# Kernel tuning notes

Measured on AMD Instinct MI355X. Metric: run time of the kernel, lower is better.

## Reference

```python
import jax, jax.numpy as jnp
import numpy as np

MUL0, MUL1, SCALARS_OUT = 16, 16, 128
L0, L1 = MUL0, MUL1 * 3            # 16, 48
PATH_NUMEL = MUL0 * MUL1 * SCALARS_OUT  # 32768 per path, two paths
EPS = 1e-5
# e3nn normalization: irrep_normalization='component' -> alpha = dim(ir_out) = 1;
# path_normalization='element' -> divide by sum over paths to same output of mul1*mul2 = 256+256 = 512.
PATH_COEFF = 1.0 / np.sqrt(512.0)
CG_110 = 1.0 / np.sqrt(3.0)  # wigner_3j(1,1,0)[i,j] = delta_ij/sqrt(3) (unit Frobenius norm)


def layer_norm(x, g, b):
    mu = jnp.mean(x, axis=-1, keepdims=True)
    var = jnp.mean(jnp.square(x - mu), axis=-1, keepdims=True)
    return (x - mu) * jax.lax.rsqrt(var + EPS) * g + b


def ff_block(x, g, b, w1, w2, b2):
    # LayerNorm -> Linear(no bias) -> SiLU -> Linear(bias); residual=False in both uses
    h = jax.nn.silu(layer_norm(x, g, b) @ w1)
    return h @ w2 + b2


def setup_inputs() -> dict:
    key = jax.random.key(0)
    ks = jax.random.split(key, 8)
    N = 2048
    return {
        "x": jax.random.normal(ks[0], (N, L0 + L1), dtype=jnp.float32),
        "we_ln_g": jnp.ones((L0,), jnp.float32),
        "we_ln_b": jnp.zeros((L0,), jnp.float32),
        "we_w1": jax.random.normal(ks[1], (L0, 4 * L0), jnp.float32) / np.sqrt(L0),
        "we_w2": jax.random.normal(ks[2], (4 * L0, 2 * PATH_NUMEL), jnp.float32) / np.sqrt(4 * L0),
        "we_b2": jnp.zeros((2 * PATH_NUMEL,), jnp.float32),
        "om_ln_g": jnp.ones((SCALARS_OUT,), jnp.float32),
        "om_ln_b": jnp.zeros((SCALARS_OUT,), jnp.float32),
        "om_w1": jax.random.normal(ks[3], (SCALARS_OUT, 4 * SCALARS_OUT), jnp.float32) / np.sqrt(SCALARS_OUT),
        "om_w2": jax.random.normal(ks[4], (4 * SCALARS_OUT, 1), jnp.float32) / np.sqrt(4 * SCALARS_OUT),
        "om_b2": jnp.zeros((1,), jnp.float32),
    }


def reference(x, we_ln_g, we_ln_b, we_w1, we_w2, we_b2,
              om_ln_g, om_ln_b, om_w1, om_w2, om_b2):
    N = x.shape[0]
    feats = x[:, :L0]                       # [N, 16] scalars (0e)
    x1 = x[:, L0:].reshape(N, MUL1, 3)      # [N, 16, 3] vectors (1o)

    # per-sample tensor-product weights (shared_weights=False)
    w = ff_block(feats, we_ln_g, we_ln_b, we_w1, we_w2, we_b2)  # [N, 65536]
    w0 = w[:, :PATH_NUMEL].reshape(N, MUL0, MUL0, SCALARS_OUT)
    w1 = w[:, PATH_NUMEL:].reshape(N, MUL1, MUL1, SCALARS_OUT)

    # path 0: 0e x 0e -> 0e  (uvw)
    o0 = jnp.einsum('nu,nv,nuvw->nw', feats, feats, w0)
    # path 1: 1o x 1o -> 0e  (uvw, CG = delta_ij/sqrt(3))
    o1 = jnp.einsum('nui,nvi,nuvw->nw', x1, x1, w1) * CG_110
    tp_out = PATH_COEFF * (o0 + o1)          # [N, 128]

    return ff_block(tp_out, om_ln_g, om_ln_b, om_w1, om_w2, om_b2)  # [N, 1]
```

## Files before the change

### kernel.cpp

```cpp
#include <hip/hip_runtime.h>
#include <hip/hip_bf16.h>
#include <cstdint>

#define EPS 1e-5f
#define PATH_COEFF 0.04419417382415922f
#define CG110     0.5773502691896258f

typedef __bf16 v8bf __attribute__((ext_vector_type(8)));
typedef float  v4f  __attribute__((ext_vector_type(4)));
typedef _Float16 v4h __attribute__((ext_vector_type(4)));

static __device__ __forceinline__ unsigned short f2bf(float x){
    unsigned int u = __builtin_bit_cast(unsigned int, x);
    u += 0x7fffu + ((u >> 16) & 1u);
    return (unsigned short)(u >> 16);
}
static __device__ __forceinline__ unsigned short f2h(float x){
    return __builtin_bit_cast(unsigned short, (_Float16)x);
}

__global__ __launch_bounds__(256)
void k_pre(const float* __restrict__ w2, const float* __restrict__ b2,
           unsigned short* __restrict__ Vt2,
           const float* __restrict__ om_w1, unsigned short* __restrict__ w1t,
           const float* __restrict__ x, const float* __restrict__ lng,
           const float* __restrict__ lnb, const float* __restrict__ we_w1,
           unsigned short* __restrict__ Q2, float* __restrict__ Ht, int N)
{
    __shared__ __align__(16) unsigned short tile[32][128];
    int b = blockIdx.x;
    int t = threadIdx.x;

    if (b < 260){
        int k    = b >> 2;
        int slab = b & 3;
        const float* srcbase = (k < 64) ? (w2 + (size_t)k * 65536) : b2;
        for (int chunk = 0; chunk < 4; ++chunk){
            int pbase = slab*128 + chunk*32;
            #pragma unroll
            for (int i = 0; i < 4; ++i){
                int g = t + 256*i;
                int ploc = g >> 5, c4 = g & 31;
                const float4 v = *(const float4*)(srcbase + (size_t)(pbase + ploc)*128 + c4*4);
                unsigned int w0 = (unsigned)f2bf(v.x) | ((unsigned)f2bf(v.y) << 16);
                unsigned int w1 = (unsigned)f2bf(v.z) | ((unsigned)f2bf(v.w) << 16);
                *(uint2*)&tile[ploc][c4*4] = make_uint2(w0, w1);
            }
            __syncthreads();
            int w = t & 127, h = t >> 7;
            int ps = slab*4 + chunk;
            unsigned int words[8];
            #pragma unroll
            for (int g2 = 0; g2 < 8; ++g2)
                words[g2] = (unsigned)tile[h*16 + g2*2][w] | ((unsigned)tile[h*16 + g2*2 + 1][w] << 16);
            unsigned short* dq0 = Vt2 + (((size_t)(k*16 + ps)*4 + 2*h    )*128 + w)*8;
            unsigned short* dq1 = Vt2 + (((size_t)(k*16 + ps)*4 + 2*h + 1)*128 + w)*8;
            *(uint4*)dq0 = make_uint4(words[0], words[1], words[2], words[3]);
            *(uint4*)dq1 = make_uint4(words[4], words[5], words[6], words[7]);
            __syncthreads();
        }
    } else if (b < 264){
        int j0 = (b - 260) * 128;
        for (int chunk = 0; chunk < 4; ++chunk){
            #pragma unroll
            for (int i = 0; i < 4; ++i){
                int g = t + 256*i;
                int wloc = g >> 5, c4 = g & 31;
                int w = chunk*32 + wloc;
                const float4 v = *(const float4*)(om_w1 + (size_t)w*512 + j0 + c4*4);
                unsigned int a = (unsigned)f2bf(v.x) | ((unsigned)f2bf(v.y) << 16);
                unsigned int bb = (unsigned)f2bf(v.z) | ((unsigned)f2bf(v.w) << 16);
                *(uint2*)&tile[wloc][c4*4] = make_uint2(a, bb);
            }
            __syncthreads();
            int jl = t & 127, h = t >> 7;
            unsigned int words[8];
            #pragma unroll
            for (int g2 = 0; g2 < 8; ++g2)
                words[g2] = (unsigned)tile[h*16 + g2*2][jl] | ((unsigned)tile[h*16 + g2*2 + 1][jl] << 16);
            unsigned short* dst = w1t + (size_t)(j0 + jl)*128 + chunk*32 + h*16;
            *(uint4*)dst       = make_uint4(words[0], words[1], words[2], words[3]);
            *(uint4*)(dst + 8) = make_uint4(words[4], words[5], words[6], words[7]);
            __syncthreads();
        }
    } else {
        int wv = t >> 6, lane = t & 63;
        int row = (b - 264)*4 + wv;
        const float* xr = x + (size_t)row * 64;
        float f[16]; float mu = 0.f;
        #pragma unroll
        for (int u = 0; u < 16; ++u){ f[u] = xr[u]; mu += f[u]; }
        mu *= (1.f/16.f);
        float var = 0.f;
        #pragma unroll
        for (int u = 0; u < 16; ++u){ float d = f[u] - mu; var += d*d; }
        var *= (1.f/16.f);
        float inv = rsqrtf(var + EPS);
        float lnf[16];
        #pragma unroll
        for (int u = 0; u < 16; ++u) lnf[u] = (f[u]-mu)*inv*lng[u] + lnb[u];
        float h1 = 0.f;
        #pragma unroll
        for (int u = 0; u < 16; ++u) h1 += lnf[u] * we_w1[u*64 + lane];
        float h = h1 / (1.f + expf(-h1));
        Ht[(size_t)lane * N + row] = h;
        if (lane == 0) Ht[(size_t)64 * N + row] = 1.f;

        union { unsigned short qs[8]; uint4 v; } qu;
        #pragma unroll
        for (int j = 0; j < 8; ++j){
            int p = lane*8 + j;
            float q;
            if (p < 256){
                int u = p >> 4, v = p & 15;
                q = PATH_COEFF * f[u] * f[v];
            } else {
                int pp = p - 256;
                int u = pp >> 4, v = pp & 15;
                const float* ya = xr + 16 + u*3;
                const float* yb = xr + 16 + v*3;
                q = (PATH_COEFF * CG110) * (ya[0]*yb[0] + ya[1]*yb[1] + ya[2]*yb[2]);
            }
            qu.qs[j] = f2bf(q);
        }
        int rb = row >> 6, r64 = row & 63;
        int ps = lane >> 2, quad4 = lane & 3;
        *(uint4*)(Q2 + (((size_t)(rb*16 + ps)*4 + quad4)*64 + r64)*8) = qu.v;
    }
}

__global__ __launch_bounds__(256, 4)
void k_main(const unsigned short* __restrict__ Q2, const unsigned short* __restrict__ Vt2,
            const float* __restrict__ Ht, unsigned short* __restrict__ partial, int N)
{
    __shared__ __align__(16) unsigned short stile[4][64*72];
    int g = blockIdx.x & 7;
    int j = blockIdx.x >> 3;
    int kb, mb;
    if (j < 128){ mb = j >> 3; kb = g*8 + (j & 7); }
    else { if (g != 0) return; mb = j - 128; kb = 64; }

    int tid  = threadIdx.x;
    int lane = tid & 63, wv = tid >> 6;
    int r2 = wv >> 1, c2 = wv & 1;
    int quad = lane >> 4, l16 = lane & 15;
    int rowbase = mb*128 + r2*64;
    int rb = rowbase >> 6;
    int wbase = c2*64;

    const unsigned short* aroot = Q2  + (size_t)rb*32768 + quad*512  + l16*8;
    const unsigned short* broot = Vt2 + (size_t)kb*65536 + quad*1024 + (wbase + l16)*8;

    v4f acc[4][4];
    #pragma unroll
    for (int m=0;m<4;++m)
      #pragma unroll
      for (int n=0;n<4;++n)
        #pragma unroll
        for (int r=0;r<4;++r) acc[m][n][r] = 0.f;

    #pragma unroll 4
    for (int ps = 0; ps < 16; ++ps){
        const unsigned short* ap = aroot + ps*2048;
        const unsigned short* bp = broot + ps*4096;
        v8bf a[4], bb[4];
        #pragma unroll
        for (int m=0;m<4;++m) a[m]  = *(const v8bf*)(ap + m*128);
        #pragma unroll
        for (int n=0;n<4;++n) bb[n] = *(const v8bf*)(bp + n*128);
        #pragma unroll
        for (int m=0;m<4;++m)
          #pragma unroll
          for (int n=0;n<4;++n)
            acc[m][n] = __builtin_amdgcn_mfma_f32_16x16x32_bf16(a[m], bb[n], acc[m][n], 0, 0, 0);
    }

    const float* hp = Ht + (size_t)kb*N + rowbase + quad*4;
    unsigned short* my = stile[wv];
    #pragma unroll
    for (int m=0;m<4;++m){
        v4f hv = *(const v4f*)(hp + m*16);
        #pragma unroll
        for (int n=0;n<4;++n)
          #pragma unroll
          for (int r=0;r<4;++r)
            my[(m*16 + quad*4 + r)*72 + n*16 + l16] = f2h(hv[r]*acc[m][n][r]);
    }
    unsigned short* gp = partial + ((size_t)(mb*65 + kb))*16384
                                 + (size_t)(r2*64)*128 + wbase;
    #pragma unroll
    for (int i = 0; i < 8; ++i){
        int row = i*8 + (lane >> 3);
        int c16 = (lane & 7)*8;
        uint4 v = *(const uint4*)&my[row*72 + c16];
        *(uint4*)(gp + (size_t)row*128 + c16) = v;
    }
}

__global__ __launch_bounds__(128)
void k_red(const unsigned short* __restrict__ partial, const float* __restrict__ g,
           const float* __restrict__ b, unsigned short* __restrict__ lnf, int N)
{
    int t = threadIdx.x;
    int row = blockIdx.x * 8 + (t >> 4);
    int w8  = (t & 15) * 8;
    int mb  = row >> 7, rin = row & 127;

    const unsigned short* p0 = partial + (size_t)mb*65*16384 + (size_t)rin*128 + w8;

    float s[8];
    #pragma unroll
    for (int j = 0; j < 8; ++j) s[j] = 0.f;

    #pragma unroll 13
    for (int sl = 0; sl < 65; ++sl){
        uint4 raw = *(const uint4*)(p0 + (size_t)sl*16384);
        union { uint4 u; _Float16 h[8]; } cv; cv.u = raw;
        #pragma unroll
        for (int j = 0; j < 8; ++j) s[j] += (float)cv.h[j];
    }

    float sum = 0.f, sq = 0.f;
    #pragma unroll
    for (int j = 0; j < 8; ++j){ sum += s[j]; sq += s[j]*s[j]; }
    #pragma unroll
    for (int off = 8; off > 0; off >>= 1){
        sum += __shfl_xor(sum, off, 16);
        sq  += __shfl_xor(sq,  off, 16);
    }
    float mu  = sum * (1.f/128.f);
    float var = sq * (1.f/128.f) - mu*mu;
    float inv = rsqrtf(var + EPS);
    unsigned short o[8];
    #pragma unroll
    for (int j = 0; j < 8; ++j)
        o[j] = f2bf((s[j]-mu)*inv*g[w8+j] + b[w8+j]);
    *(uint4*)(lnf + (size_t)row*128 + w8) = *(uint4*)o;
}

__global__ __launch_bounds__(256)
void k_mlp2(const unsigned short* __restrict__ lnf, const unsigned short* __restrict__ w1t,
            const float* __restrict__ w2, const float* __restrict__ b2,
            float* __restrict__ out, int N)
{
    __shared__ float red2[4][32];
    int tid = threadIdx.x, lane = tid & 63, wv = tid >> 6;
    int quad = lane >> 4, l16 = lane & 15;
    int rowbase = blockIdx.x * 32;
    int jbase = wv * 128;

    v4f acc[2][8];
    #pragma unroll
    for (int m=0;m<2;++m)
      #pragma unroll
      for (int n=0;n<8;++n)
        #pragma unroll
        for (int r=0;r<4;++r) acc[m][n][r] = 0.f;

    #pragma unroll
    for (int ps = 0; ps < 4; ++ps){
        v8bf a[2], bb[8];
        #pragma unroll
        for (int m=0;m<2;++m)
            a[m]  = *(const v8bf*)(lnf + (size_t)(rowbase + m*16 + l16)*128 + ps*32 + quad*8);
        #pragma unroll
        for (int n=0;n<8;++n)
            bb[n] = *(const v8bf*)(w1t + (size_t)(jbase + n*16 + l16)*128 + ps*32 + quad*8);
        #pragma unroll
        for (int m=0;m<2;++m)
          #pragma unroll
          for (int n=0;n<8;++n)
            acc[m][n] = __builtin_amdgcn_mfma_f32_16x16x32_bf16(a[m], bb[n], acc[m][n], 0, 0, 0);
    }

    float w2v[8];
    #pragma unroll
    for (int n=0;n<8;++n) w2v[n] = w2[jbase + n*16 + l16];

    #pragma unroll
    for (int m=0;m<2;++m){
        #pragma unroll
        for (int r=0;r<4;++r){
            float s = 0.f;
            #pragma unroll
            for (int n=0;n<8;++n){
                float v = acc[m][n][r];
                s += (v / (1.f + expf(-v))) * w2v[n];
            }
            #pragma unroll
            for (int off=8; off>0; off>>=1) s += __shfl_xor(s, off, 16);
            if (l16 == 0) red2[wv][m*16 + quad*4 + r] = s;
        }
    }
    __syncthreads();
    if (tid < 32)
        out[rowbase + tid] = red2[0][tid] + red2[1][tid] + red2[2][tid] + red2[3][tid] + b2[0];
}

extern "C" void kernel_launch(void* const* d_in, const int* in_sizes, int n_in,
                              void* d_out, int out_size, void* d_ws, size_t ws_size,
                              hipStream_t stream)
{
    const float* x     = (const float*)d_in[0];
    const float* we_g  = (const float*)d_in[1];
    const float* we_b  = (const float*)d_in[2];
    const float* we_w1 = (const float*)d_in[3];
    const float* we_w2 = (const float*)d_in[4];
    const float* we_b2 = (const float*)d_in[5];
    const float* om_g  = (const float*)d_in[6];
    const float* om_b  = (const float*)d_in[7];
    const float* om_w1 = (const float*)d_in[8];
    const float* om_w2 = (const float*)d_in[9];
    const float* om_b2 = (const float*)d_in[10];

    int N  = in_sizes[0] / 64;

    char* ws = (char*)d_ws;
    size_t offV = 0;
    size_t szV  = (size_t)65*16*4*128*8*2;
    size_t offQ = offV + szV;
    size_t szQ  = (size_t)N*512*2;
    size_t offH = offQ + szQ;
    size_t szH  = (size_t)65*N*4;
    size_t offP = offH + szH;
    size_t szP  = (size_t)65*N*128*2;
    size_t offL = offP + szP;
    size_t szL  = (size_t)N*128*2;
    size_t offW = offL + szL;

    unsigned short* Vt2 = (unsigned short*)(ws + offV);
    unsigned short* Q2  = (unsigned short*)(ws + offQ);
    float* Ht           = (float*)(ws + offH);
    unsigned short* Par = (unsigned short*)(ws + offP);
    unsigned short* Lnf = (unsigned short*)(ws + offL);
    unsigned short* W1t = (unsigned short*)(ws + offW);
    float* out = (float*)d_out;

    hipLaunchKernelGGL(k_pre,  dim3(264 + N/4), dim3(256), 0, stream,
                       we_w2, we_b2, Vt2, om_w1, W1t, x, we_g, we_b, we_w1, Q2, Ht, N);
    hipLaunchKernelGGL(k_main, dim3(144*8),     dim3(256), 0, stream, Q2, Vt2, Ht, Par, N);
    hipLaunchKernelGGL(k_red,  dim3(N/8),       dim3(128), 0, stream, Par, om_g, om_b, Lnf, N);
    hipLaunchKernelGGL(k_mlp2, dim3(N/32),      dim3(256), 0, stream, Lnf, W1t, om_w2, om_b2, out, N);
}
```

Measured before the change: 137.9 us.

## Process two hidden units per k_main block to halve partial-sum traffic

Each k_main block now computes two k slices (two hidden units) with separate accumulators that share the same A fragments. It combines them with their Ht scales before writing a single fp16 partial, so the partial buffer and the k_red reduction shrink from 65 to 33 slices. This cuts global writes and reads of partials and reuses A loads. In exchange it doubles accumulator registers, lowers the occupancy target to 2 blocks, and launches fewer blocks.

```diff
diff --git a/kernel.cpp b/kernel.cpp
--- a/kernel.cpp
+++ b/kernel.cpp
@@ -129,16 +129,16 @@
     }
 }
 
-__global__ __launch_bounds__(256, 4)
+__global__ __launch_bounds__(256, 2)
 void k_main(const unsigned short* __restrict__ Q2, const unsigned short* __restrict__ Vt2,
             const float* __restrict__ Ht, unsigned short* __restrict__ partial, int N)
 {
     __shared__ __align__(16) unsigned short stile[4][64*72];
     int g = blockIdx.x & 7;
     int j = blockIdx.x >> 3;
-    int kb, mb;
-    if (j < 128){ mb = j >> 3; kb = g*8 + (j & 7); }
-    else { if (g != 0) return; mb = j - 128; kb = 64; }
+    int kg, mb;
+    if (j < 64){ mb = j >> 2; kg = g*4 + (j & 3); }
+    else { if (g != 0) return; mb = j - 64; kg = 32; }
 
     int tid  = threadIdx.x;
     int lane = tid & 63, wv = tid >> 6;
@@ -148,45 +148,61 @@
     int rb = rowbase >> 6;
     int wbase = c2*64;
 
-    const unsigned short* aroot = Q2  + (size_t)rb*32768 + quad*512  + l16*8;
-    const unsigned short* broot = Vt2 + (size_t)kb*65536 + quad*1024 + (wbase + l16)*8;
-
-    v4f acc[4][4];
+    int k0 = kg*2;
+    int k1 = (kg == 32) ? 64 : k0 + 1;
+    float sel = (kg == 32) ? 0.f : 1.f;
+
+    const unsigned short* aroot  = Q2  + (size_t)rb*32768 + quad*512  + l16*8;
+    const unsigned short* broot0 = Vt2 + (size_t)k0*65536 + quad*1024 + (wbase + l16)*8;
+    const unsigned short* broot1 = Vt2 + (size_t)k1*65536 + quad*1024 + (wbase + l16)*8;
+
+    v4f accA[4][4], accB[4][4];
     #pragma unroll
     for (int m=0;m<4;++m)
       #pragma unroll
       for (int n=0;n<4;++n)
         #pragma unroll
-        for (int r=0;r<4;++r) acc[m][n][r] = 0.f;
-
-    #pragma unroll 4
+        for (int r=0;r<4;++r){ accA[m][n][r] = 0.f; accB[m][n][r] = 0.f; }
+
+    #pragma unroll 2
     for (int ps = 0; ps < 16; ++ps){
-        const unsigned short* ap = aroot + ps*2048;
-        const unsigned short* bp = broot + ps*4096;
-        v8bf a[4], bb[4];
-        #pragma unroll
-        for (int m=0;m<4;++m) a[m]  = *(const v8bf*)(ap + m*128);
-        #pragma unroll
-        for (int n=0;n<4;++n) bb[n] = *(const v8bf*)(bp + n*128);
+        const unsigned short* ap  = aroot  + ps*2048;
+        const unsigned short* bp0 = broot0 + ps*4096;
+        const unsigned short* bp1 = broot1 + ps*4096;
+        v8bf a[4], b0[4], b1[4];
+        #pragma unroll
+        for (int m=0;m<4;++m) a[m]  = *(const v8bf*)(ap  + m*128);
+        #pragma unroll
+        for (int n=0;n<4;++n) b0[n] = *(const v8bf*)(bp0 + n*128);
+        #pragma unroll
+        for (int n=0;n<4;++n) b1[n] = *(const v8bf*)(bp1 + n*128);
         #pragma unroll
         for (int m=0;m<4;++m)
           #pragma unroll
           for (int n=0;n<4;++n)
-            acc[m][n] = __builtin_amdgcn_mfma_f32_16x16x32_bf16(a[m], bb[n], acc[m][n], 0, 0, 0);
-    }
-
-    const float* hp = Ht + (size_t)kb*N + rowbase + quad*4;
+            accA[m][n] = __builtin_amdgcn_mfma_f32_16x16x32_bf16(a[m], b0[n], accA[m][n], 0, 0, 0);
+        #pragma unroll
+        for (int m=0;m<4;++m)
+          #pragma unroll
+          for (int n=0;n<4;++n)
+            accB[m][n] = __builtin_amdgcn_mfma_f32_16x16x32_bf16(a[m], b1[n], accB[m][n], 0, 0, 0);
+    }
+
+    const float* hp0 = Ht + (size_t)k0*N + rowbase + quad*4;
+    const float* hp1 = Ht + (size_t)k1*N + rowbase + quad*4;
     unsigned short* my = stile[wv];
     #pragma unroll
     for (int m=0;m<4;++m){
-        v4f hv = *(const v4f*)(hp + m*16);
+        v4f h0 = *(const v4f*)(hp0 + m*16);
+        v4f h1 = *(const v4f*)(hp1 + m*16);
         #pragma unroll
         for (int n=0;n<4;++n)
           #pragma unroll
           for (int r=0;r<4;++r)
-            my[(m*16 + quad*4 + r)*72 + n*16 + l16] = f2h(hv[r]*acc[m][n][r]);
-    }
-    unsigned short* gp = partial + ((size_t)(mb*65 + kb))*16384
+            my[(m*16 + quad*4 + r)*72 + n*16 + l16] =
+                f2h(h0[r]*accA[m][n][r] + sel*h1[r]*accB[m][n][r]);
+    }
+    unsigned short* gp = partial + ((size_t)(mb*33 + kg))*16384
                                  + (size_t)(r2*64)*128 + wbase;
     #pragma unroll
     for (int i = 0; i < 8; ++i){
@@ -206,14 +222,14 @@
     int w8  = (t & 15) * 8;
     int mb  = row >> 7, rin = row & 127;
 
-    const unsigned short* p0 = partial + (size_t)mb*65*16384 + (size_t)rin*128 + w8;
+    const unsigned short* p0 = partial + (size_t)mb*33*16384 + (size_t)rin*128 + w8;
 
     float s[8];
     #pragma unroll
     for (int j = 0; j < 8; ++j) s[j] = 0.f;
 
-    #pragma unroll 13
-    for (int sl = 0; sl < 65; ++sl){
+    #pragma unroll 11
+    for (int sl = 0; sl < 33; ++sl){
         uint4 raw = *(const uint4*)(p0 + (size_t)sl*16384);
         union { uint4 u; _Float16 h[8]; } cv; cv.u = raw;
         #pragma unroll
@@ -323,7 +339,7 @@
     size_t offH = offQ + szQ;
     size_t szH  = (size_t)65*N*4;
     size_t offP = offH + szH;
-    size_t szP  = (size_t)65*N*128*2;
+    size_t szP  = (size_t)(N/128)*33*16384*2;
     size_t offL = offP + szP;
     size_t szL  = (size_t)N*128*2;
     size_t offW = offL + szL;
@@ -338,7 +354,7 @@
 
     hipLaunchKernelGGL(k_pre,  dim3(264 + N/4), dim3(256), 0, stream,
                        we_w2, we_b2, Vt2, om_w1, W1t, x, we_g, we_b, we_w1, Q2, Ht, N);
-    hipLaunchKernelGGL(k_main, dim3(144*8),     dim3(256), 0, stream, Q2, Vt2, Ht, Par, N);
+    hipLaunchKernelGGL(k_main, dim3(80*8),      dim3(256), 0, stream, Q2, Vt2, Ht, Par, N);
     hipLaunchKernelGGL(k_red,  dim3(N/8),       dim3(128), 0, stream, Par, om_g, om_b, Lnf, N);
     hipLaunchKernelGGL(k_mlp2, dim3(N/32),      dim3(256), 0, stream, Lnf, W1t, om_w2, om_b2, out, N);
 }
```

Result: no change. 135.7 us (-1.6%).
